# Kernel tuning notes

Measured on AMD Instinct MI355X. Metric: run time of the kernel, lower is better.

## Reference

```python
import jax, jax.numpy as jnp
import numpy as np

EPS = 1e-8  # torch.nn.CosineSimilarity default eps


def setup_inputs() -> dict:
    key = jax.random.key(0)
    k1, k2 = jax.random.split(key)
    input1 = jax.random.normal(k1, (8192, 128), dtype=jnp.float32)
    input2 = jax.random.normal(k2, (8192, 128), dtype=jnp.float32)
    return {"input1": input1, "input2": input2}


def reference(input1, input2):
    # Pairwise cosine similarity [N, M]:
    # sim = <x, y> / max(||x|| * ||y||, eps)  (matches torch CosineSimilarity)
    dots = jnp.einsum("nd,md->nm", input1, input2)          # [N, M]
    n1 = jnp.linalg.norm(input1, axis=-1)                    # [N]
    n2 = jnp.linalg.norm(input2, axis=-1)                    # [M]
    denom = jnp.maximum(n1[:, None] * n2[None, :], EPS)      # [N, M]
    return dots / denom
```

## Files before the change

### kernel.cpp

```cpp
#include <hip/hip_runtime.h>
#include <hip/hip_bf16.h>

#define NROWS 8192
#define DDIM 128

typedef __attribute__((ext_vector_type(8))) short bf16x8;
typedef __attribute__((ext_vector_type(4))) float f32x4;

__global__ __launch_bounds__(256) void prep_kernel(
    const float* __restrict__ in1, const float* __restrict__ in2,
    __hip_bfloat16* __restrict__ Apk, __hip_bfloat16* __restrict__ Bpk,
    float* __restrict__ rn1, float* __restrict__ rn2) {
  int gw = (blockIdx.x * 256 + threadIdx.x) >> 6;
  int l = threadIdx.x & 63;
  int row;
  const float* src;
  char* dstbase;
  float* nrm;
  if (gw < NROWS) {
    row = gw;
    src = in1 + (size_t)row * DDIM;
    dstbase = (char*)Apk;
    nrm = rn1 + row;
  } else {
    row = gw - NROWS;
    src = in2 + (size_t)row * DDIM;
    dstbase = (char*)Bpk;
    nrm = rn2 + row;
  }
  float2 v = ((const float2*)src)[l];
  float s = v.x * v.x + v.y * v.y;
  __hip_bfloat162 h;
  h.x = __float2bfloat16(v.x);
  h.y = __float2bfloat16(v.y);

  int rb = row >> 4, ri = row & 15;
  int sk = l >> 4;
  int q2 = (l & 15) >> 2;
  int j2 = l & 3;
  char* dst = dstbase + (size_t)(rb * 4 + sk) * 1024 + ri * 64 + q2 * 16 + j2 * 4;
  *(__hip_bfloat162*)dst = h;

#pragma unroll
  for (int off = 1; off < 64; off <<= 1) s += __shfl_xor(s, off);
  if (l == 0) *nrm = 1.0f / sqrtf(s);
}

__device__ inline void async_load16(const void* g, void* l) {
  __builtin_amdgcn_global_load_lds(
      (const __attribute__((address_space(1))) void*)g,
      (__attribute__((address_space(3))) void*)l, 16, 0, 0);
}

__global__ __launch_bounds__(256, 2) void cos_gemm(
    const __hip_bfloat16* __restrict__ Apk, const __hip_bfloat16* __restrict__ Bpk,
    const float* __restrict__ rn1, const float* __restrict__ rn2,
    float* __restrict__ out) {
  __shared__ char lds[64 * 1024];
  char* lA = lds;
  char* lB = lds + 32 * 1024;

  const int tid = threadIdx.x;
  const int l = tid & 63;
  const int w = tid >> 6;
  const int q = l >> 4;
  const int c16 = l & 15;
  const int wr = w >> 1, wc = w & 1;

  int wg = blockIdx.x;
  int xcd = wg & 7;
  int c = wg >> 3;
  const int brow = (xcd * 8 + (c >> 6)) * 128;
  const int bcol = (c & 63) * 128;

  const char* Ag = (const char*)Apk + (size_t)(brow >> 4) * 4096;
  const char* Bg = (const char*)Bpk + (size_t)(bcol >> 4) * 4096;
#pragma unroll
  for (int i = 0; i < 8; ++i) {
    int f = w * 8 + i;
    async_load16(Ag + f * 1024 + l * 16, lA + f * 1024);
    async_load16(Bg + f * 1024 + l * 16, lB + f * 1024);
  }
  __syncthreads();

  const int laneoff = c16 * 64 + q * 16;
  f32x4 acc[4][4] = {};
#pragma unroll
  for (int s = 0; s < 4; ++s) {
    bf16x8 af[4], bfr[4];
#pragma unroll
    for (int m = 0; m < 4; ++m) {
      af[m]  = *(const bf16x8*)(lA + ((wr * 4 + m) * 4 + s) * 1024 + laneoff);
      bfr[m] = *(const bf16x8*)(lB + ((wc * 4 + m) * 4 + s) * 1024 + laneoff);
    }
#pragma unroll
    for (int m = 0; m < 4; ++m)
#pragma unroll
      for (int n = 0; n < 4; ++n)
        acc[m][n] =
            __builtin_amdgcn_mfma_f32_16x16x32_bf16(bfr[n], af[m], acc[m][n], 0, 0, 0);
  }

  float r1v[4];
#pragma unroll
  for (int m = 0; m < 4; ++m) r1v[m] = rn1[brow + wr * 64 + m * 16 + c16];
  float4 r2v[4];
#pragma unroll
  for (int n = 0; n < 4; ++n)
    r2v[n] = *(const float4*)&rn2[bcol + wc * 64 + n * 16 + q * 4];

#pragma unroll
  for (int m = 0; m < 4; ++m) {
    size_t rowoff = (size_t)(brow + wr * 64 + m * 16 + c16) * NROWS;
#pragma unroll
    for (int n = 0; n < 4; ++n) {
      f32x4 v;
      v[0] = acc[m][n][0] * r1v[m] * r2v[n].x;
      v[1] = acc[m][n][1] * r1v[m] * r2v[n].y;
      v[2] = acc[m][n][2] * r1v[m] * r2v[n].z;
      v[3] = acc[m][n][3] * r1v[m] * r2v[n].w;
      *(f32x4*)(out + rowoff + bcol + wc * 64 + n * 16 + q * 4) = v;
    }
  }
}

extern "C" void kernel_launch(void* const* d_in, const int* in_sizes, int n_in,
                              void* d_out, int out_size, void* d_ws, size_t ws_size,
                              hipStream_t stream) {
  const float* in1 = (const float*)d_in[0];
  const float* in2 = (const float*)d_in[1];
  float* out = (float*)d_out;
  char* ws = (char*)d_ws;

  __hip_bfloat16* Apk = (__hip_bfloat16*)(ws);
  __hip_bfloat16* Bpk = (__hip_bfloat16*)(ws + (size_t)NROWS * DDIM * 2);
  float* rn1 = (float*)(ws + (size_t)NROWS * DDIM * 4);
  float* rn2 = (float*)(ws + (size_t)NROWS * DDIM * 4 + NROWS * 4);

  prep_kernel<<<dim3(16384 / 4), 256, 0, stream>>>(in1, in2, Apk, Bpk, rn1, rn2);
  cos_gemm<<<dim3(4096), 256, 0, stream>>>(Apk, Bpk, rn1, rn2, out);
}
```

Before: 78.60 us.

## Pre-normalize rows in prep and loop over column tiles with double-buffered B

The prep kernel now scales each row by its reciprocal norm before the bf16 conversion, so the GEMM epilogue no longer loads norms or multiplies. The GEMM launches 512 persistent-style blocks, each holding its A fragments in registers and iterating over 8 column tiles, double-buffering B tiles in LDS with async loads overlapped with the MFMA and store work. The intent is to amortize A loads and launch overhead and to overlap B loads with the output-store-bound epilogue. Risks include fewer blocks for latency hiding, extra register pressure from the held A fragments, and a subtle change in rounding because normalization now happens before bf16 quantization. The eps clamp was already absent, so zero-norm rows are unchanged.

```diff
diff --git a/kernel.cpp b/kernel.cpp
--- a/kernel.cpp
+++ b/kernel.cpp
@@ -9,30 +9,30 @@
 
 __global__ __launch_bounds__(256) void prep_kernel(
     const float* __restrict__ in1, const float* __restrict__ in2,
-    __hip_bfloat16* __restrict__ Apk, __hip_bfloat16* __restrict__ Bpk,
-    float* __restrict__ rn1, float* __restrict__ rn2) {
+    __hip_bfloat16* __restrict__ Apk, __hip_bfloat16* __restrict__ Bpk) {
   int gw = (blockIdx.x * 256 + threadIdx.x) >> 6;
   int l = threadIdx.x & 63;
   int row;
   const float* src;
   char* dstbase;
-  float* nrm;
   if (gw < NROWS) {
     row = gw;
     src = in1 + (size_t)row * DDIM;
     dstbase = (char*)Apk;
-    nrm = rn1 + row;
   } else {
     row = gw - NROWS;
     src = in2 + (size_t)row * DDIM;
     dstbase = (char*)Bpk;
-    nrm = rn2 + row;
   }
   float2 v = ((const float2*)src)[l];
   float s = v.x * v.x + v.y * v.y;
+#pragma unroll
+  for (int off = 1; off < 64; off <<= 1) s += __shfl_xor(s, off);
+  float rn = 1.0f / sqrtf(s);
+
   __hip_bfloat162 h;
-  h.x = __float2bfloat16(v.x);
-  h.y = __float2bfloat16(v.y);
+  h.x = __float2bfloat16(v.x * rn);
+  h.y = __float2bfloat16(v.y * rn);
 
   int rb = row >> 4, ri = row & 15;
   int sk = l >> 4;
@@ -40,10 +40,6 @@
   int j2 = l & 3;
   char* dst = dstbase + (size_t)(rb * 4 + sk) * 1024 + ri * 64 + q2 * 16 + j2 * 4;
   *(__hip_bfloat162*)dst = h;
-
-#pragma unroll
-  for (int off = 1; off < 64; off <<= 1) s += __shfl_xor(s, off);
-  if (l == 0) *nrm = 1.0f / sqrtf(s);
 }
 
 __device__ inline void async_load16(const void* g, void* l) {
@@ -54,11 +50,10 @@
 
 __global__ __launch_bounds__(256, 2) void cos_gemm(
     const __hip_bfloat16* __restrict__ Apk, const __hip_bfloat16* __restrict__ Bpk,
-    const float* __restrict__ rn1, const float* __restrict__ rn2,
     float* __restrict__ out) {
   __shared__ char lds[64 * 1024];
-  char* lA = lds;
-  char* lB = lds + 32 * 1024;
+  char* lB0 = lds;
+  char* lB1 = lds + 32 * 1024;
 
   const int tid = threadIdx.x;
   const int l = tid & 63;
@@ -67,59 +62,71 @@
   const int c16 = l & 15;
   const int wr = w >> 1, wc = w & 1;
 
-  int wg = blockIdx.x;
-  int xcd = wg & 7;
-  int c = wg >> 3;
-  const int brow = (xcd * 8 + (c >> 6)) * 128;
-  const int bcol = (c & 63) * 128;
+  const int bid = blockIdx.x;
+  const int strip = bid & 7;
+  const int brow = (bid >> 3) * 128;
+  const int bcol0 = strip * 1024;
 
-  const char* Ag = (const char*)Apk + (size_t)(brow >> 4) * 4096;
-  const char* Bg = (const char*)Bpk + (size_t)(bcol >> 4) * 4096;
+  const int laneoff = c16 * 64 + q * 16;
+
+  const char* Ap = (const char*)Apk + ((size_t)(brow >> 4) + wr * 4) * 4096;
+  bf16x8 afr[4][4];
 #pragma unroll
-  for (int i = 0; i < 8; ++i) {
-    int f = w * 8 + i;
-    async_load16(Ag + f * 1024 + l * 16, lA + f * 1024);
-    async_load16(Bg + f * 1024 + l * 16, lB + f * 1024);
+  for (int m = 0; m < 4; ++m)
+#pragma unroll
+    for (int s = 0; s < 4; ++s)
+      afr[m][s] = *(const bf16x8*)(Ap + (m * 4 + s) * 1024 + laneoff);
+
+  const char* Bp = (const char*)Bpk;
+  {
+    const char* src = Bp + (size_t)(bcol0 >> 4) * 4096;
+#pragma unroll
+    for (int i = 0; i < 8; ++i)
+      async_load16(src + i * 4096 + tid * 16, lB0 + i * 4096 + tid * 16);
   }
   __syncthreads();
 
-  const int laneoff = c16 * 64 + q * 16;
-  f32x4 acc[4][4] = {};
+#pragma unroll 2
+  for (int t = 0; t < 8; ++t) {
+    char* cur = (t & 1) ? lB1 : lB0;
+    char* nxt = (t & 1) ? lB0 : lB1;
+
+    if (t < 7) {
+      const char* src = Bp + (size_t)((bcol0 + (t + 1) * 128) >> 4) * 4096;
 #pragma unroll
-  for (int s = 0; s < 4; ++s) {
-    bf16x8 af[4], bfr[4];
+      for (int i = 0; i < 8; ++i)
+        async_load16(src + i * 4096 + tid * 16, nxt + i * 4096 + tid * 16);
+    }
+
+    f32x4 acc[4][4] = {};
+#pragma unroll
+    for (int s = 0; s < 4; ++s) {
+      bf16x8 bfr[4];
+#pragma unroll
+      for (int n = 0; n < 4; ++n)
+        bfr[n] = *(const bf16x8*)(cur + ((wc * 4 + n) * 4 + s) * 1024 + laneoff);
+#pragma unroll
+      for (int m = 0; m < 4; ++m)
+#pragma unroll
+        for (int n = 0; n < 4; ++n)
+          acc[m][n] = __builtin_amdgcn_mfma_f32_16x16x32_bf16(
+              bfr[n], afr[m][s], acc[m][n], 0, 0, 0);
+    }
+
+    const int bcol = bcol0 + t * 128;
 #pragma unroll
     for (int m = 0; m < 4; ++m) {
-      af[m]  = *(const bf16x8*)(lA + ((wr * 4 + m) * 4 + s) * 1024 + laneoff);
-      bfr[m] = *(const bf16x8*)(lB + ((wc * 4 + m) * 4 + s) * 1024 + laneoff);
-    }
-#pragma unroll
-    for (int m = 0; m < 4; ++m)
+      size_t rowoff = (size_t)(brow + wr * 64 + m * 16 + c16) * NROWS;
 #pragma unroll
       for (int n = 0; n < 4; ++n)
-        acc[m][n] =
-            __builtin_amdgcn_mfma_f32_16x16x32_bf16(bfr[n], af[m], acc[m][n], 0, 0, 0);
-  }
+        *(f32x4*)(out + rowoff + bcol + wc * 64 + n * 16 + q * 4) = acc[m][n];
+    }
 
-  float r1v[4];
-#pragma unroll
-  for (int m = 0; m < 4; ++m) r1v[m] = rn1[brow + wr * 64 + m * 16 + c16];
-  float4 r2v[4];
-#pragma unroll
-  for (int n = 0; n < 4; ++n)
-    r2v[n] = *(const float4*)&rn2[bcol + wc * 64 + n * 16 + q * 4];
-
-#pragma unroll
-  for (int m = 0; m < 4; ++m) {
-    size_t rowoff = (size_t)(brow + wr * 64 + m * 16 + c16) * NROWS;
-#pragma unroll
-    for (int n = 0; n < 4; ++n) {
-      f32x4 v;
-      v[0] = acc[m][n][0] * r1v[m] * r2v[n].x;
-      v[1] = acc[m][n][1] * r1v[m] * r2v[n].y;
-      v[2] = acc[m][n][2] * r1v[m] * r2v[n].z;
-      v[3] = acc[m][n][3] * r1v[m] * r2v[n].w;
-      *(f32x4*)(out + rowoff + bcol + wc * 64 + n * 16 + q * 4) = v;
+    if (t < 7) {
+      asm volatile("s_waitcnt vmcnt(16)" ::: "memory");
+      __builtin_amdgcn_sched_barrier(0);
+      __builtin_amdgcn_s_barrier();
+      __builtin_amdgcn_sched_barrier(0);
     }
   }
 }
@@ -134,9 +141,7 @@
 
   __hip_bfloat16* Apk = (__hip_bfloat16*)(ws);
   __hip_bfloat16* Bpk = (__hip_bfloat16*)(ws + (size_t)NROWS * DDIM * 2);
-  float* rn1 = (float*)(ws + (size_t)NROWS * DDIM * 4);
-  float* rn2 = (float*)(ws + (size_t)NROWS * DDIM * 4 + NROWS * 4);
 
-  prep_kernel<<<dim3(16384 / 4), 256, 0, stream>>>(in1, in2, Apk, Bpk, rn1, rn2);
-  cos_gemm<<<dim3(4096), 256, 0, stream>>>(Apk, Bpk, rn1, rn2, out);
+  prep_kernel<<<dim3(16384 / 4), 256, 0, stream>>>(in1, in2, Apk, Bpk);
+  cos_gemm<<<dim3(512), 256, 0, stream>>>(Apk, Bpk, out);
 }
```

After: 69.48 us. 11.6% less time.
